# Kernel optimization log

Hardware: AMD Instinct MI355X
Metric: run time of the kernel (lower is better)

Reference implementation:

```python
import jax, jax.numpy as jnp
import numpy as np

NU, NB, NI = 50000, 20000, 100000
D = 64
NUM_LAYERS = 2
CORE_K = 3
PAD = NI  # padding index for bundle_items
BATCH, NCAND = 2048, 2
MAXDEG = 50
E_UB, E_UI, E_BI = 800000, 1000000, 1200000
N_UB, N_UI, N_BI = NU + NB, NU + NI, NB + NI


def setup_inputs():
    key = jax.random.key(0)
    ks = jax.random.split(key, 24)
    f = jnp.float32
    inp = {
        'users_feature': jax.random.normal(ks[0], (NU, D), f) * 0.1,
        'bundles_feature': jax.random.normal(ks[1], (NB, D), f) * 0.1,
        'items_feature': jax.random.normal(ks[2], (NI, D), f) * 0.1,
        'mlp_core_w1': jax.random.normal(ks[3], (2, 32), f) * 0.1,
        'mlp_core_b1': jnp.zeros((32,), f),
        'mlp_core_w2': jax.random.normal(ks[4], (32, 1), f) * 0.1,
        'mlp_core_b2': jnp.zeros((1,), f),
        'mlp_syn_w1': jax.random.normal(ks[5], (2 * D, D), f) * 0.05,
        'mlp_syn_b1': jnp.zeros((D,), f),
        'mlp_syn_w2': jax.random.normal(ks[6], (D, D), f) * 0.05,
        'mlp_syn_b2': jnp.zeros((D,), f),
        'ub_val': jax.random.uniform(ks[7], (E_UB,), f) * 0.2,
        'ui_val': jax.random.uniform(ks[8], (E_UI,), f) * 0.2,
        'bi_val': jax.random.uniform(ks[9], (E_BI,), f) * 0.2,
        'users': jax.random.randint(ks[10], (BATCH,), 0, NU),
        'bundles': jax.random.randint(ks[11], (BATCH, NCAND), 0, NB),
        'ub_row': jax.random.randint(ks[12], (E_UB,), 0, N_UB, jnp.int32),
        'ub_col': jax.random.randint(ks[13], (E_UB,), 0, N_UB, jnp.int32),
        'ui_row': jax.random.randint(ks[14], (E_UI,), 0, N_UI, jnp.int32),
        'ui_col': jax.random.randint(ks[15], (E_UI,), 0, N_UI, jnp.int32),
        'bi_row': jax.random.randint(ks[16], (E_BI,), 0, N_BI, jnp.int32),
        'bi_col': jax.random.randint(ks[17], (E_BI,), 0, N_BI, jnp.int32),
        'bundle_items': jax.random.randint(ks[18], (NB, MAXDEG), 0, NI + 1),
    }
    return inp


def spmm(row, col, val, x):
    # y = A @ x for COO sparse A: gather source rows, scale, scatter-add to dest rows
    return jax.ops.segment_sum(val[:, None] * x[col], row, num_segments=x.shape[0])


def propagate(row, col, val, feat_a, feat_b):
    f = jnp.concatenate([feat_a, feat_b], axis=0)
    acc = f
    for _ in range(NUM_LAYERS):
        f = spmm(row, col, val, f)
        acc = acc + f
    m = acc / (NUM_LAYERS + 1)  # mean over hop outputs
    return m[:feat_a.shape[0]], m[feat_a.shape[0]:]


def core_fringe_scores(users, bundles, reps, bundle_items,
                       cw1, cb1, cw2, cb2, sw1, sb1, sw2, sb2):
    UB_u, UB_b, UI_u, UI_i, BI_b, BI_i = reps
    B, C = bundles.shape
    users_exp = jnp.repeat(users, C)            # [B*C]
    bundles_flat = bundles.reshape(-1)          # [B*C]
    bbi = bundle_items[bundles_flat]            # [B*C, M]
    mask = bbi != PAD
    zero = jnp.zeros((1, D), UI_i.dtype)
    items_ui = jnp.concatenate([UI_i, zero], 0)[bbi]  # [B*C, M, D]
    items_bi = jnp.concatenate([BI_i, zero], 0)[bbi]
    u_ui = UI_u[users_exp]                      # [B*C, D]
    b_bi = BI_b[bundles_flat]
    r_UI = jnp.einsum('nd,nmd->nm', u_ui, items_ui)
    r_BI = jnp.einsum('nd,nmd->nm', b_bi, items_bi)
    x = jnp.stack([r_UI, r_BI], axis=-1)        # [B*C, M, 2]
    h = jax.nn.relu(x @ cw1 + cb1)              # dropout omitted (eval-mode determinism)
    logits = (h @ cw2 + cb2)[..., 0]
    logits = jnp.where(mask, logits, -jnp.inf)
    pi = jax.nn.softmax(logits, axis=1)
    k = min(CORE_K, bbi.shape[1])
    topv, topi = jax.lax.top_k(pi, k)
    topp = topv / (topv.sum(axis=1, keepdims=True) + 1e-10)
    core_emb = jnp.take_along_axis(items_ui, topi[:, :, None], axis=1)
    h_core = (core_emb * topp[:, :, None]).sum(axis=1)
    n = pi.shape[0]
    is_core = jnp.zeros(pi.shape, bool).at[jnp.arange(n)[:, None], topi].set(True)
    is_fringe = mask & ~is_core
    fr = is_fringe[:, :, None].astype(items_ui.dtype)
    fringe_sum = (items_ui * fr).sum(axis=1)
    fringe_cnt = jnp.maximum(is_fringe.sum(axis=1, keepdims=True).astype(items_ui.dtype), 1.0)
    h_fringe = fringe_sum / fringe_cnt
    syn = jnp.concatenate([h_core, h_fringe], axis=1)
    phi = jax.nn.relu(syn @ sw1 + sb1) @ sw2 + sb2
    hat_e_BI = h_core + phi
    user_final = jnp.concatenate([u_ui, UB_u[users_exp]], axis=1)
    bundle_final = jnp.concatenate([UB_b[bundles_flat], hat_e_BI], axis=1)
    scores = (user_final * bundle_final).sum(axis=1)
    return scores.reshape(B, C)


def reference(users_feature, bundles_feature, items_feature,
              mlp_core_w1, mlp_core_b1, mlp_core_w2, mlp_core_b2,
              mlp_syn_w1, mlp_syn_b1, mlp_syn_w2, mlp_syn_b2,
              ub_val, ui_val, bi_val,
              users, bundles, ub_row, ub_col, ui_row, ui_col,
              bi_row, bi_col, bundle_items):
    UB_u, UB_b = propagate(ub_row, ub_col, ub_val, users_feature, bundles_feature)
    UI_u, UI_i = propagate(ui_row, ui_col, ui_val, users_feature, items_feature)
    BI_b, BI_i = propagate(bi_row, bi_col, bi_val, bundles_feature, items_feature)
    reps = (UB_u, UB_b, UI_u, UI_i, BI_b, BI_i)
    scores = core_fringe_scores(users, bundles, reps, bundle_items,
                                mlp_core_w1, mlp_core_b1, mlp_core_w2, mlp_core_b2,
                                mlp_syn_w1, mlp_syn_b1, mlp_syn_w2, mlp_syn_b2)
    # BPR loss: -log(sigmoid(pos - neg)) == softplus(neg - pos)
    bpr_loss = jnp.mean(jax.nn.softplus(scores[:, 1:] - scores[:, 0:1]))
    return bpr_loss
```

## Files before the change

kernel.cpp:

```cpp
#include <hip/hip_runtime.h>
#include <math.h>

constexpr int D = 64;
constexpr int NU = 50000, NB = 20000, NI = 100000;
constexpr int BATCH = 2048, NCAND = 2, MAXDEG = 50, CORE_K = 3;
constexpr int PAD_IDX = NI;
constexpr int N_UB = NU + NB, N_UI = NU + NI, N_BI = NB + NI;
constexpr int N_TOT = N_UB + N_UI + N_BI;
constexpr int OFF1 = N_UB;
constexpr int OFF2 = N_UB + N_UI;
constexpr int CAP = 48;
constexpr float VAL_SCALE = 16383.0f / 0.2f;
constexpr float VAL_INV   = 0.2f / 16383.0f;

constexpr int GB_BASE = NU;
constexpr int GI_BASE = NU + NB;
constexpr int NGF = NU + NB + NI;

constexpr int BSHIFT = 9;
constexpr int BROWS  = 1 << BSHIFT;
constexpr int NBUCK  = (N_TOT + BROWS - 1) >> BSHIFT;
constexpr int BCAP   = 6144;
constexpr int P1_EPT = 16;
constexpr int P1_TPB = 256;
constexpr int P1_EPB = P1_EPT * P1_TPB;

constexpr int L2_NCB = BATCH * NCAND;
constexpr int L2_SLOTS = 2 * NI + 2 * BATCH + 2 * L2_NCB;
constexpr int S_UBU = 2 * NI;
constexpr int S_UIU = 2 * NI + BATCH;
constexpr int S_UBB = 2 * NI + 2 * BATCH;
constexpr int S_BIB = S_UBB + L2_NCB;

constexpr int MARK_A_BLOCKS = (L2_NCB * MAXDEG + 255) / 256;
constexpr int MARK_B_ROWS   = BATCH + L2_NCB;

__device__ __forceinline__ float wave_sum64(float v) {
#pragma unroll
    for (int off = 32; off > 0; off >>= 1) v += __shfl_down(v, off);
    return v;
}

__device__ __forceinline__ float bflo(unsigned u) { return __uint_as_float(u << 16); }
__device__ __forceinline__ float bfhi(unsigned u) { return __uint_as_float(u & 0xFFFF0000u); }
__device__ __forceinline__ unsigned short f2bf(float f) {
    unsigned u = __float_as_uint(f);
    u += 0x7FFF + ((u >> 16) & 1);
    return (unsigned short)(u >> 16);
}
__device__ __forceinline__ unsigned pack2(float a, float b) {
    return (unsigned)f2bf(a) | ((unsigned)f2bf(b) << 16);
}
__device__ __forceinline__ float bf1(const unsigned short* p) {
    return __uint_as_float(((unsigned)*p) << 16);
}

__device__ __forceinline__ void edge_decode(unsigned u, int& col, float& v) {
    col = (int)(u & 0x3FFFFu);
    v = (float)(u >> 18) * VAL_INV;
}

__global__ __launch_bounds__(256) void k_bin1cvt(
    const int* __restrict__ r0, const int* __restrict__ c0,
    const float* __restrict__ v0,
    const int* __restrict__ r1, const int* __restrict__ c1,
    const float* __restrict__ v1,
    const int* __restrict__ r2, const int* __restrict__ c2,
    const float* __restrict__ v2,
    int e0, int e1, int e2, int nb1,
    int* __restrict__ bcnt, uint2* __restrict__ stage,
    const float* __restrict__ uf, const float* __restrict__ bf,
    const float* __restrict__ itf, unsigned short* __restrict__ gt) {
    const int t = threadIdx.x;
    if ((int)blockIdx.x >= nb1) {
        size_t i = (size_t)(blockIdx.x - nb1) * 256 + t;
        if (i >= (size_t)NGF * 16) return;
        int row = (int)(i >> 4);
        int q = ((int)i & 15) * 4;
        const float* src;
        if (row < GB_BASE)      src = uf  + (size_t)row * D;
        else if (row < GI_BASE) src = bf  + (size_t)(row - GB_BASE) * D;
        else                    src = itf + (size_t)(row - GI_BASE) * D;
        float4 v = *(const float4*)(src + q);
        ushort4 o;
        o.x = f2bf(v.x); o.y = f2bf(v.y); o.z = f2bf(v.z); o.w = f2bf(v.w);
        *(ushort4*)(gt + (size_t)row * D + q) = o;
        return;
    }
    __shared__ int s_hist[NBUCK];
    __shared__ unsigned s_base[NBUCK];
    __shared__ uint2 s_ed[P1_EPB];
    const int etot = e0 + e1 + e2;
    const int i0 = blockIdx.x * P1_EPB + t;
    for (int l = t; l < NBUCK; l += P1_TPB) s_hist[l] = 0;
    __syncthreads();
#pragma unroll
    for (int k = 0; k < P1_EPT; ++k) {
        int i = i0 + k * P1_TPB;
        uint2 ed = make_uint2(0u, 0xFFFFFFFFu);
        if (i < etot) {
            int r, g; float v;
            if (i < e0)           { r = r0[i]; g = c0[i]; v = v0[i]; }
            else if (i < e0 + e1) { int j = i - e0; r = r1[j] + OFF1;
                                    int c = c1[j]; g = (c < NU) ? c : c + NB; v = v1[j]; }
            else                  { int j = i - e0 - e1; r = r2[j] + OFF2;
                                    g = c2[j] + NU; v = v2[j]; }
            unsigned q = (unsigned)fminf(v * VAL_SCALE + 0.5f, 16383.0f);
            int lo = atomicAdd(&s_hist[r >> BSHIFT], 1);
            ed = make_uint2((q << 18) | (unsigned)g,
                            (unsigned)r | ((unsigned)lo << 19));
        }
        s_ed[k * P1_TPB + t] = ed;
    }
    __syncthreads();
    for (int l = t; l < NBUCK; l += P1_TPB)
        s_base[l] = (unsigned)atomicAdd(&bcnt[l], s_hist[l]);
    __syncthreads();
#pragma unroll
    for (int k = 0; k < P1_EPT; ++k) {
        uint2 e = s_ed[k * P1_TPB + t];
        if (e.y == 0xFFFFFFFFu) continue;
        unsigned r = e.y & 0x7FFFFu;
        unsigned b = r >> BSHIFT;
        unsigned slot = s_base[b] + (e.y >> 19);
        if (slot < (unsigned)BCAP)
            stage[(size_t)b * BCAP + slot] = make_uint2(e.x, r);
    }
}

__global__ __launch_bounds__(1024) void k_bin2(
    const int* __restrict__ bcnt, const uint2* __restrict__ stage,
    int* __restrict__ cnt, unsigned* __restrict__ cv) {
    __shared__ unsigned lcv[BROWS][CAP];
    __shared__ int s_c[BROWS];
    const int b = blockIdx.x;
    const int t = threadIdx.x;
    if (t < BROWS) s_c[t] = 0;
    __syncthreads();
    int nb = bcnt[b]; if (nb > BCAP) nb = BCAP;
    const uint2* sp = stage + (size_t)b * BCAP;
    const int rbase = b << BSHIFT;
    for (int i = t; i < nb; i += 1024) {
        uint2 e = sp[i];
        int rl = (int)e.y - rbase;
        int slot = atomicAdd(&s_c[rl], 1);
        if (slot < CAP) lcv[rl][slot] = e.x;
    }
    __syncthreads();
    if (t < BROWS && rbase + t < N_TOT) cnt[rbase + t] = s_c[t];
    const int g16 = t >> 4;
    const int l16 = t & 15;
#pragma unroll 1
    for (int rl = g16; rl < BROWS; rl += 64) {
        int r = rbase + rl;
        if (r >= N_TOT) continue;
        int deg = s_c[rl]; if (deg > CAP) deg = CAP;
        if (deg == 0) continue;
        int nwords = (deg + 15) & ~15;
        if (l16 * 4 < nwords) {
            uint4 w = *(const uint4*)&lcv[rl][l16 * 4];
            *(uint4*)(cv + (size_t)r * CAP + l16 * 4) = w;
        }
    }
}

__global__ __launch_bounds__(256) void k_mark(
    const int* __restrict__ users, const int* __restrict__ bundles,
    const int* __restrict__ bundle_items,
    const int* __restrict__ cnt, const unsigned* __restrict__ cv,
    unsigned char* __restrict__ fS, unsigned char* __restrict__ f1,
    unsigned char* __restrict__ f2) {
    const int bid = blockIdx.x, t = threadIdx.x;
    if (bid < MARK_A_BLOCKS) {
        int i = bid * 256 + t;
        if (i < L2_NCB * MAXDEG) {
            int it = bundle_items[(size_t)bundles[i / MAXDEG] * MAXDEG + (i % MAXDEG)];
            if (it != PAD_IDX) fS[it] = 1;
        }
        return;
    }
    int q = (bid - MARK_A_BLOCKS) * 256 + t;
    if (q >= MARK_B_ROWS) return;
    int r; unsigned char* f;
    if (q < BATCH) { r = OFF1 + users[q];          f = f1; }
    else           { r = OFF2 + bundles[q - BATCH]; f = f2; }
    int deg = cnt[r]; if (deg > CAP) deg = CAP;
    const unsigned* ce = cv + (size_t)r * CAP;
    for (int j = 0; j < deg; ++j) {
        int g = (int)(ce[j] & 0x3FFFFu);
        if (g >= GI_BASE) f[g - GI_BASE] = 1;
    }
}

__global__ __launch_bounds__(256) void k_spmm_l1(
    const int* __restrict__ cnt, const unsigned* __restrict__ cv,
    const unsigned short* __restrict__ gt,
    const unsigned char* __restrict__ f1, const unsigned char* __restrict__ f2,
    unsigned short* __restrict__ y1) {
    int r = blockIdx.x * 32 + (threadIdx.x >> 3);
    int t = threadIdx.x & 7;
    if (r >= N_TOT) return;
    if (r >= OFF1 + NU && r < OFF2) { if (!f1[r - OFF1 - NU]) return; }
    else if (r >= OFF2 + NB)        { if (!f2[r - OFF2 - NB]) return; }
    int deg = cnt[r]; if (deg > CAP) deg = CAP;
    const unsigned* ce = cv + (size_t)r * CAP;
    float a[8];
#pragma unroll
    for (int k = 0; k < 8; ++k) a[k] = 0.f;
    int j = 0;
    for (; j + 3 < deg; j += 4) {
        int c[4]; float v[4]; uint4 u[4];
#pragma unroll
        for (int k = 0; k < 4; ++k) edge_decode(ce[j + k], c[k], v[k]);
#pragma unroll
        for (int k = 0; k < 4; ++k)
            u[k] = *(const uint4*)(gt + (((size_t)c[k]) << 6) + t * 8);
#pragma unroll
        for (int k = 0; k < 4; ++k) {
            a[0] = fmaf(v[k], bflo(u[k].x), a[0]); a[1] = fmaf(v[k], bfhi(u[k].x), a[1]);
            a[2] = fmaf(v[k], bflo(u[k].y), a[2]); a[3] = fmaf(v[k], bfhi(u[k].y), a[3]);
            a[4] = fmaf(v[k], bflo(u[k].z), a[4]); a[5] = fmaf(v[k], bfhi(u[k].z), a[5]);
            a[6] = fmaf(v[k], bflo(u[k].w), a[6]); a[7] = fmaf(v[k], bfhi(u[k].w), a[7]);
        }
    }
    for (; j < deg; ++j) {
        int c0; float v0;
        edge_decode(ce[j], c0, v0);
        uint4 u0 = *(const uint4*)(gt + (((size_t)c0) << 6) + t * 8);
        a[0] = fmaf(v0, bflo(u0.x), a[0]); a[1] = fmaf(v0, bfhi(u0.x), a[1]);
        a[2] = fmaf(v0, bflo(u0.y), a[2]); a[3] = fmaf(v0, bfhi(u0.y), a[3]);
        a[4] = fmaf(v0, bflo(u0.z), a[4]); a[5] = fmaf(v0, bfhi(u0.z), a[5]);
        a[6] = fmaf(v0, bflo(u0.w), a[6]); a[7] = fmaf(v0, bfhi(u0.w), a[7]);
    }
    uint4 o;
    o.x = pack2(a[0], a[1]); o.y = pack2(a[2], a[3]);
    o.z = pack2(a[4], a[5]); o.w = pack2(a[6], a[7]);
    *(uint4*)(y1 + ((size_t)r << 6) + t * 8) = o;
}

__global__ __launch_bounds__(256) void k_spmm_l2(
    const int* __restrict__ cnt, const unsigned* __restrict__ cv,
    const int* __restrict__ users, const int* __restrict__ bundles,
    const unsigned short* __restrict__ y1, const unsigned short* __restrict__ gt,
    const unsigned char* __restrict__ fS,
    unsigned short* __restrict__ xc) {
    int s = blockIdx.x * 32 + (threadIdx.x >> 3);
    int t = threadIdx.x & 7;
    if (s >= L2_SLOTS) return;
    int r, g, sec;
    if (s < NI)                { if (!fS[s]) return;
                                 r = OFF1 + NU + s;        g = GI_BASE + s;        sec = 1; }
    else if (s < 2 * NI)       { int i = s - NI; if (!fS[i]) return;
                                 r = OFF2 + NB + i;        g = GI_BASE + i;        sec = 2; }
    else {
        int q = s - 2 * NI;
        if (q < BATCH)            { int u = users[q];             r = u;         g = u;            sec = 0; }
        else if (q < 2 * BATCH)   { int u = users[q - BATCH];     r = OFF1 + u;  g = u;            sec = 1; }
        else if (q < S_BIB - 2 * NI) { int b = bundles[q - 2 * BATCH];
                                    r = NU + b;    g = GB_BASE + b;  sec = 0; }
        else                      { int b = bundles[q - (S_BIB - 2 * NI)];
                                    r = OFF2 + b;  g = GB_BASE + b;  sec = 2; }
    }
    auto y1row = [&](int gg) -> int {
        if (sec == 0) return gg;
        if (sec == 2) return OFF2 - GB_BASE + gg;
        return OFF1 + ((gg < NU) ? gg : gg - NB);
    };
    int deg = cnt[r]; if (deg > CAP) deg = CAP;
    const unsigned* ce = cv + (size_t)r * CAP;
    float a[8];
#pragma unroll
    for (int k = 0; k < 8; ++k) a[k] = 0.f;
    int j = 0;
    for (; j + 3 < deg; j += 4) {
        int c[4]; float v[4]; uint4 u[4];
#pragma unroll
        for (int k = 0; k < 4; ++k) edge_decode(ce[j + k], c[k], v[k]);
#pragma unroll
        for (int k = 0; k < 4; ++k)
            u[k] = *(const uint4*)(y1 + (((size_t)y1row(c[k])) << 6) + t * 8);
#pragma unroll
        for (int k = 0; k < 4; ++k) {
            a[0] = fmaf(v[k], bflo(u[k].x), a[0]); a[1] = fmaf(v[k], bfhi(u[k].x), a[1]);
            a[2] = fmaf(v[k], bflo(u[k].y), a[2]); a[3] = fmaf(v[k], bfhi(u[k].y), a[3]);
            a[4] = fmaf(v[k], bflo(u[k].z), a[4]); a[5] = fmaf(v[k], bfhi(u[k].z), a[5]);
            a[6] = fmaf(v[k], bflo(u[k].w), a[6]); a[7] = fmaf(v[k], bfhi(u[k].w), a[7]);
        }
    }
    for (; j < deg; ++j) {
        int c0; float v0;
        edge_decode(ce[j], c0, v0);
        uint4 u0 = *(const uint4*)(y1 + (((size_t)y1row(c0)) << 6) + t * 8);
        a[0] = fmaf(v0, bflo(u0.x), a[0]); a[1] = fmaf(v0, bfhi(u0.x), a[1]);
        a[2] = fmaf(v0, bflo(u0.y), a[2]); a[3] = fmaf(v0, bfhi(u0.y), a[3]);
        a[4] = fmaf(v0, bflo(u0.z), a[4]); a[5] = fmaf(v0, bfhi(u0.z), a[5]);
        a[6] = fmaf(v0, bflo(u0.w), a[6]); a[7] = fmaf(v0, bfhi(u0.w), a[7]);
    }
    uint4 fx = *(const uint4*)(gt + ((size_t)g << 6) + t * 8);
    uint4 yx = *(const uint4*)(y1 + ((size_t)r << 6) + t * 8);
    constexpr float k3 = 1.0f / 3.0f;
    float o[8];
    o[0] = (bflo(fx.x) + bflo(yx.x) + a[0]) * k3;
    o[1] = (bfhi(fx.x) + bfhi(yx.x) + a[1]) * k3;
    o[2] = (bflo(fx.y) + bflo(yx.y) + a[2]) * k3;
    o[3] = (bfhi(fx.y) + bfhi(yx.y) + a[3]) * k3;
    o[4] = (bflo(fx.z) + bflo(yx.z) + a[4]) * k3;
    o[5] = (bfhi(fx.z) + bfhi(yx.z) + a[5]) * k3;
    o[6] = (bflo(fx.w) + bflo(yx.w) + a[6]) * k3;
    o[7] = (bfhi(fx.w) + bfhi(yx.w) + a[7]) * k3;
    uint4 w;
    w.x = pack2(o[0], o[1]); w.y = pack2(o[2], o[3]);
    w.z = pack2(o[4], o[5]); w.w = pack2(o[6], o[7]);
    *(uint4*)(xc + ((size_t)s << 6) + t * 8) = w;
}

__global__ __launch_bounds__(256) void k_score(
    const int* __restrict__ bundles,
    const int* __restrict__ bundle_items,
    const unsigned short* __restrict__ xc,
    const float* __restrict__ cw1, const float* __restrict__ cb1,
    const float* __restrict__ cw2, const float* __restrict__ cb2,
    const float* __restrict__ sw1, const float* __restrict__ sb1,
    const float* __restrict__ sw2, const float* __restrict__ sb2,
    float* __restrict__ accum, unsigned* __restrict__ tick,
    float* __restrict__ out) {
    const int t  = threadIdx.x;
    const int wv = t >> 6;
    const int ln = t & 63;
    const int n  = blockIdx.x * 4 + wv;
    const int g8 = ln >> 3;
    const int l8 = ln & 7;
    const int uq = n >> 1;
    const int b = bundles[n];

    __shared__ unsigned sh_it[4][MAXDEG][32];
    __shared__ float sh_r[4][2][MAXDEG];
    __shared__ float sh_syn[4][2 * D];
    __shared__ float sh_h1[4][D];
    __shared__ float sh_sc[4];

    int my_idx = (ln < MAXDEG) ? bundle_items[(size_t)b * MAXDEG + ln] : PAD_IDX;
    unsigned long long vmask = __ballot(my_idx != PAD_IDX);

    uint4 ufr = *(const uint4*)(xc + (((size_t)(S_UIU + uq)) << 6) + l8 * 8);
    uint4 bfr = *(const uint4*)(xc + (((size_t)(S_BIB + n)) << 6) + l8 * 8);
    float uf0 = bflo(ufr.x), uf1 = bfhi(ufr.x), uf2 = bflo(ufr.y), uf3 = bfhi(ufr.y);
    float uf4 = bflo(ufr.z), uf5 = bfhi(ufr.z), uf6 = bflo(ufr.w), uf7 = bfhi(ufr.w);
    float bf0 = bflo(bfr.x), bf1_ = bfhi(bfr.x), bf2 = bflo(bfr.y), bf3 = bfhi(bfr.y);
    float bf4 = bflo(bfr.z), bf5 = bfhi(bfr.z), bf6 = bflo(bfr.w), bf7 = bfhi(bfr.w);

    for (int iter = 0; iter < (MAXDEG + 7) / 8; ++iter) {
        int m = iter * 8 + g8;
        if (m >= MAXDEG) continue;
        int it = __shfl(my_idx, m);
        uint4 iu = make_uint4(0, 0, 0, 0);
        float pu = 0.f, pb = 0.f;
        if (it != PAD_IDX) {
            iu = *(const uint4*)(xc + (((size_t)it) << 6) + l8 * 8);
            uint4 ib = *(const uint4*)(xc + (((size_t)(NI + it)) << 6) + l8 * 8);
            pu = uf0 * bflo(iu.x) + uf1 * bfhi(iu.x) + uf2 * bflo(iu.y) + uf3 * bfhi(iu.y)
               + uf4 * bflo(iu.z) + uf5 * bfhi(iu.z) + uf6 * bflo(iu.w) + uf7 * bfhi(iu.w);
            pb = bf0 * bflo(ib.x) + bf1_ * bfhi(ib.x) + bf2 * bflo(ib.y) + bf3 * bfhi(ib.y)
               + bf4 * bflo(ib.z) + bf5 * bfhi(ib.z) + bf6 * bflo(ib.w) + bf7 * bfhi(ib.w);
        }
        *(uint4*)&sh_it[wv][m][l8 * 4] = iu;
#pragma unroll
        for (int off = 4; off > 0; off >>= 1) {
            pu += __shfl_down(pu, off, 8);
            pb += __shfl_down(pb, off, 8);
        }
        if (l8 == 0) { sh_r[wv][0][m] = pu; sh_r[wv][1][m] = pb; }
    }
    __builtin_amdgcn_wave_barrier();

    float logit = -INFINITY;
    if (ln < MAXDEG && my_idx != PAD_IDX) {
        float rU = sh_r[wv][0][ln], rB = sh_r[wv][1][ln];
        float acc = cb2[0];
#pragma unroll
        for (int j = 0; j < 32; ++j) {
            float h = fmaf(rU, cw1[j], fmaf(rB, cw1[32 + j], cb1[j]));
            h = fmaxf(h, 0.f);
            acc = fmaf(h, cw2[j], acc);
        }
        logit = acc;
    }

    float mx = logit;
#pragma unroll
    for (int off = 32; off > 0; off >>= 1) mx = fmaxf(mx, __shfl_xor(mx, off));
    float e = expf(logit - mx);
    float sm = e;
#pragma unroll
    for (int off = 32; off > 0; off >>= 1) sm += __shfl_xor(sm, off);
    float p = e / sm;

    int ti[CORE_K]; float tp[CORE_K];
    float vsel = p;
#pragma unroll
    for (int k = 0; k < CORE_K; ++k) {
        float vv = vsel; int ii = ln;
#pragma unroll
        for (int off = 32; off > 0; off >>= 1) {
            float v2 = __shfl_xor(vv, off);
            int   i2 = __shfl_xor(ii, off);
            if (v2 > vv || (v2 == vv && i2 < ii)) { vv = v2; ii = i2; }
        }
        ti[k] = ii; tp[k] = vv;
        if (ln == ii) vsel = -1.f;
    }
    float tinv = 1.f / (tp[0] + tp[1] + tp[2] + 1e-10f);
    tp[0] *= tinv; tp[1] *= tinv; tp[2] *= tinv;

    int ti0 = ti[0], ti1 = ti[1], ti2 = ti[2];
    const int ui_w = ln >> 1;
    const bool hi = (ln & 1);
    auto feat = [&](int m) -> float {
        unsigned w = sh_it[wv][m][ui_w];
        return hi ? bfhi(w) : bflo(w);
    };
    float hcore = feat(ti0) * tp[0] + feat(ti1) * tp[1] + feat(ti2) * tp[2];
    float fsum = 0.f;
#pragma unroll 10
    for (int m = 0; m < MAXDEG; ++m) fsum += feat(m);
    int fcnt = __popcll(vmask);
#pragma unroll
    for (int k = 0; k < CORE_K; ++k) {
        if ((vmask >> ti[k]) & 1ull) { fsum -= feat(ti[k]); fcnt--; }
    }
    float hfr = fsum / fmaxf((float)fcnt, 1.f);
    sh_syn[wv][ln] = hcore;
    sh_syn[wv][D + ln] = hfr;
    __builtin_amdgcn_wave_barrier();

    float h1 = sb1[ln];
#pragma unroll 8
    for (int k0 = 0; k0 < 32; ++k0) {
        float4 s4 = *(const float4*)&sh_syn[wv][k0 * 4];
        h1 = fmaf(s4.x, sw1[(k0 * 4 + 0) * D + ln], h1);
        h1 = fmaf(s4.y, sw1[(k0 * 4 + 1) * D + ln], h1);
        h1 = fmaf(s4.z, sw1[(k0 * 4 + 2) * D + ln], h1);
        h1 = fmaf(s4.w, sw1[(k0 * 4 + 3) * D + ln], h1);
    }
    sh_h1[wv][ln] = fmaxf(h1, 0.f);
    __builtin_amdgcn_wave_barrier();
    float phi = sb2[ln];
#pragma unroll 8
    for (int k0 = 0; k0 < 16; ++k0) {
        float4 s4 = *(const float4*)&sh_h1[wv][k0 * 4];
        phi = fmaf(s4.x, sw2[(k0 * 4 + 0) * D + ln], phi);
        phi = fmaf(s4.y, sw2[(k0 * 4 + 1) * D + ln], phi);
        phi = fmaf(s4.z, sw2[(k0 * 4 + 2) * D + ln], phi);
        phi = fmaf(s4.w, sw2[(k0 * 4 + 3) * D + ln], phi);
    }

    float hat = hcore + phi;
    float uui = bf1(xc + (((size_t)(S_UIU + uq)) << 6) + ln);
    float ubu = bf1(xc + (((size_t)(S_UBU + uq)) << 6) + ln);
    float ubb = bf1(xc + (((size_t)(S_UBB + n)) << 6) + ln);
    float part = wave_sum64(uui * ubb + ubu * hat);
    if (ln == 0) sh_sc[wv] = part;

    __syncthreads();
    if (t == 0) {
        float x01 = sh_sc[1] - sh_sc[0];
        float x23 = sh_sc[3] - sh_sc[2];
        float spv = fmaxf(x01, 0.f) + log1pf(expf(-fabsf(x01)))
                  + fmaxf(x23, 0.f) + log1pf(expf(-fabsf(x23)));
        atomicAdd(accum, spv * (1.0f / (float)BATCH));
        __threadfence();
        unsigned old = atomicAdd(tick, 1u);
        if (old == gridDim.x - 1) {
            __threadfence();
            float total = atomicAdd(accum, 0.0f);
            out[0] = total;
        }
    }
}

extern "C" void kernel_launch(void* const* d_in, const int* in_sizes, int n_in,
                              void* d_out, int out_size, void* d_ws, size_t ws_size,
                              hipStream_t stream) {
    const float* users_feature   = (const float*)d_in[0];
    const float* bundles_feature = (const float*)d_in[1];
    const float* items_feature   = (const float*)d_in[2];
    const float* cw1 = (const float*)d_in[3];
    const float* cb1 = (const float*)d_in[4];
    const float* cw2 = (const float*)d_in[5];
    const float* cb2 = (const float*)d_in[6];
    const float* sw1 = (const float*)d_in[7];
    const float* sb1 = (const float*)d_in[8];
    const float* sw2 = (const float*)d_in[9];
    const float* sb2 = (const float*)d_in[10];
    const float* ub_val = (const float*)d_in[11];
    const float* ui_val = (const float*)d_in[12];
    const float* bi_val = (const float*)d_in[13];
    const int* users   = (const int*)d_in[14];
    const int* bundles = (const int*)d_in[15];
    const int* ub_row = (const int*)d_in[16];
    const int* ub_col = (const int*)d_in[17];
    const int* ui_row = (const int*)d_in[18];
    const int* ui_col = (const int*)d_in[19];
    const int* bi_row = (const int*)d_in[20];
    const int* bi_col = (const int*)d_in[21];
    const int* bundle_items = (const int*)d_in[22];
    const int E_UB = in_sizes[11], E_UI = in_sizes[12], E_BI = in_sizes[13];
    const int E_TOT = E_UB + E_UI + E_BI;

    float* ws = (float*)d_ws;
    size_t off = 0;
    unsigned short* gt  = (unsigned short*)(ws + off); off += (size_t)NGF * 32;
    unsigned short* y1b = (unsigned short*)(ws + off); off += (size_t)N_TOT * 32;
    unsigned* cv  = (unsigned*)(ws + off); off += (size_t)N_TOT * CAP;
    uint2* stage = (uint2*)(ws + off);
    unsigned short* xc = (unsigned short*)(ws + off);
    off += (size_t)NBUCK * BCAP * 2;
    int*   bcnt   = (int*)(ws + off); off += NBUCK;
    unsigned* tick = (unsigned*)(ws + off); off += 1;
    float* accum  = (float*)(ws + off); off += 1;
    unsigned char* fS = (unsigned char*)(ws + off); off += NI / 4;
    unsigned char* f1 = (unsigned char*)(ws + off); off += NI / 4;
    unsigned char* f2 = (unsigned char*)(ws + off); off += NI / 4;
    int*   cnt    = (int*)(ws + off); off += N_TOT;
    if (ws_size < off * sizeof(float)) return;

    hipMemsetAsync(bcnt, 0, (NBUCK + 2) * sizeof(int) + 3 * NI, stream);

    const int nb1 = (E_TOT + P1_EPB - 1) / P1_EPB;
    const int ncvt = (int)(((size_t)NGF * 16 + 255) / 256);
    k_bin1cvt<<<nb1 + ncvt, P1_TPB, 0, stream>>>(
        ub_row, ub_col, ub_val, ui_row, ui_col, ui_val, bi_row, bi_col, bi_val,
        E_UB, E_UI, E_BI, nb1, bcnt, stage,
        users_feature, bundles_feature, items_feature, gt);

    k_bin2<<<NBUCK, 1024, 0, stream>>>(bcnt, stage, cnt, cv);

    const int nmarkB = (MARK_B_ROWS + 255) / 256;
    k_mark<<<MARK_A_BLOCKS + nmarkB, 256, 0, stream>>>(
        users, bundles, bundle_items, cnt, cv, fS, f1, f2);

    k_spmm_l1<<<(N_TOT + 31) / 32, 256, 0, stream>>>(cnt, cv, gt, f1, f2, y1b);

    k_spmm_l2<<<(L2_SLOTS + 31) / 32, 256, 0, stream>>>(
        cnt, cv, users, bundles, y1b, gt, fS, xc);

    k_score<<<(BATCH * NCAND) / 4, 256, 0, stream>>>(
        bundles, bundle_items, xc,
        cw1, cb1, cw2, cb2, sw1, sb1, sw2, sb2,
        accum, tick, (float*)d_out);
}
```

Measured before the change: 331.9 us.

## Fold marking kernel into binning kernels and halve edges per thread

Removes the separate k_mark launch. Item-set marking and user/bundle batch flags now run as extra blocks of the first binning kernel, and neighbor marking of batch rows happens inside k_bin2 from shared-memory adjacency. Edges per thread in the first pass drop from 16 to 8, which doubles the number of binning blocks. The aim is to save a launch plus a global re-read of cv/cnt, at the cost of serial per-row marking loops in k_bin2 and more global atomics on the bucket counters.

```diff
diff --git a/kernel.cpp b/kernel.cpp
--- a/kernel.cpp
+++ b/kernel.cpp
@@ -21,7 +21,7 @@
 constexpr int BROWS  = 1 << BSHIFT;
 constexpr int NBUCK  = (N_TOT + BROWS - 1) >> BSHIFT;
 constexpr int BCAP   = 6144;
-constexpr int P1_EPT = 16;
+constexpr int P1_EPT = 8;
 constexpr int P1_TPB = 256;
 constexpr int P1_EPB = P1_EPT * P1_TPB;
 
@@ -33,7 +33,7 @@
 constexpr int S_BIB = S_UBB + L2_NCB;
 
 constexpr int MARK_A_BLOCKS = (L2_NCB * MAXDEG + 255) / 256;
-constexpr int MARK_B_ROWS   = BATCH + L2_NCB;
+constexpr int MARK_D_BLOCKS = (BATCH + L2_NCB + 255) / 256;
 
 __device__ __forceinline__ float wave_sum64(float v) {
 #pragma unroll
@@ -67,13 +67,32 @@
     const float* __restrict__ v1,
     const int* __restrict__ r2, const int* __restrict__ c2,
     const float* __restrict__ v2,
-    int e0, int e1, int e2, int nb1,
+    int e0, int e1, int e2, int nb1, int nb2, int nb3,
     int* __restrict__ bcnt, uint2* __restrict__ stage,
     const float* __restrict__ uf, const float* __restrict__ bf,
-    const float* __restrict__ itf, unsigned short* __restrict__ gt) {
+    const float* __restrict__ itf, unsigned short* __restrict__ gt,
+    const int* __restrict__ users, const int* __restrict__ bundles,
+    const int* __restrict__ bundle_items,
+    unsigned char* __restrict__ fS, unsigned char* __restrict__ du,
+    unsigned char* __restrict__ db) {
     const int t = threadIdx.x;
-    if ((int)blockIdx.x >= nb1) {
-        size_t i = (size_t)(blockIdx.x - nb1) * 256 + t;
+    const int bid = (int)blockIdx.x;
+    if (bid >= nb3) {
+        int q = (bid - nb3) * 256 + t;
+        if (q < BATCH) du[users[q]] = 1;
+        else if (q < BATCH + L2_NCB) db[bundles[q - BATCH]] = 1;
+        return;
+    }
+    if (bid >= nb2) {
+        int i = (bid - nb2) * 256 + t;
+        if (i < L2_NCB * MAXDEG) {
+            int it = bundle_items[(size_t)bundles[i / MAXDEG] * MAXDEG + (i % MAXDEG)];
+            if (it != PAD_IDX) fS[it] = 1;
+        }
+        return;
+    }
+    if (bid >= nb1) {
+        size_t i = (size_t)(bid - nb1) * 256 + t;
         if (i >= (size_t)NGF * 16) return;
         int row = (int)(i >> 4);
         int q = ((int)i & 15) * 4;
@@ -91,7 +110,7 @@
     __shared__ unsigned s_base[NBUCK];
     __shared__ uint2 s_ed[P1_EPB];
     const int etot = e0 + e1 + e2;
-    const int i0 = blockIdx.x * P1_EPB + t;
+    const int i0 = bid * P1_EPB + t;
     for (int l = t; l < NBUCK; l += P1_TPB) s_hist[l] = 0;
     __syncthreads();
 #pragma unroll
@@ -130,7 +149,9 @@
 
 __global__ __launch_bounds__(1024) void k_bin2(
     const int* __restrict__ bcnt, const uint2* __restrict__ stage,
-    int* __restrict__ cnt, unsigned* __restrict__ cv) {
+    const unsigned char* __restrict__ du, const unsigned char* __restrict__ db,
+    int* __restrict__ cnt, unsigned* __restrict__ cv,
+    unsigned char* __restrict__ f1, unsigned char* __restrict__ f2) {
     __shared__ unsigned lcv[BROWS][CAP];
     __shared__ int s_c[BROWS];
     const int b = blockIdx.x;
@@ -148,6 +169,19 @@
     }
     __syncthreads();
     if (t < BROWS && rbase + t < N_TOT) cnt[rbase + t] = s_c[t];
+    if (t < BROWS) {
+        int r = rbase + t;
+        unsigned char* f = nullptr;
+        if (r >= OFF1 && r < OFF1 + NU)      { if (du[r - OFF1]) f = f1; }
+        else if (r >= OFF2 && r < OFF2 + NB) { if (db[r - OFF2]) f = f2; }
+        if (f) {
+            int deg = s_c[t]; if (deg > CAP) deg = CAP;
+            for (int j = 0; j < deg; ++j) {
+                int g = (int)(lcv[t][j] & 0x3FFFFu);
+                if (g >= GI_BASE) f[g - GI_BASE] = 1;
+            }
+        }
+    }
     const int g16 = t >> 4;
     const int l16 = t & 15;
 #pragma unroll 1
@@ -161,34 +195,6 @@
             uint4 w = *(const uint4*)&lcv[rl][l16 * 4];
             *(uint4*)(cv + (size_t)r * CAP + l16 * 4) = w;
         }
-    }
-}
-
-__global__ __launch_bounds__(256) void k_mark(
-    const int* __restrict__ users, const int* __restrict__ bundles,
-    const int* __restrict__ bundle_items,
-    const int* __restrict__ cnt, const unsigned* __restrict__ cv,
-    unsigned char* __restrict__ fS, unsigned char* __restrict__ f1,
-    unsigned char* __restrict__ f2) {
-    const int bid = blockIdx.x, t = threadIdx.x;
-    if (bid < MARK_A_BLOCKS) {
-        int i = bid * 256 + t;
-        if (i < L2_NCB * MAXDEG) {
-            int it = bundle_items[(size_t)bundles[i / MAXDEG] * MAXDEG + (i % MAXDEG)];
-            if (it != PAD_IDX) fS[it] = 1;
-        }
-        return;
-    }
-    int q = (bid - MARK_A_BLOCKS) * 256 + t;
-    if (q >= MARK_B_ROWS) return;
-    int r; unsigned char* f;
-    if (q < BATCH) { r = OFF1 + users[q];          f = f1; }
-    else           { r = OFF2 + bundles[q - BATCH]; f = f2; }
-    int deg = cnt[r]; if (deg > CAP) deg = CAP;
-    const unsigned* ce = cv + (size_t)r * CAP;
-    for (int j = 0; j < deg; ++j) {
-        int g = (int)(ce[j] & 0x3FFFFu);
-        if (g >= GI_BASE) f[g - GI_BASE] = 1;
     }
 }
 
@@ -521,23 +527,24 @@
     unsigned char* fS = (unsigned char*)(ws + off); off += NI / 4;
     unsigned char* f1 = (unsigned char*)(ws + off); off += NI / 4;
     unsigned char* f2 = (unsigned char*)(ws + off); off += NI / 4;
+    unsigned char* du = (unsigned char*)(ws + off); off += NU / 4;
+    unsigned char* db = (unsigned char*)(ws + off); off += NB / 4;
     int*   cnt    = (int*)(ws + off); off += N_TOT;
     if (ws_size < off * sizeof(float)) return;
 
-    hipMemsetAsync(bcnt, 0, (NBUCK + 2) * sizeof(int) + 3 * NI, stream);
+    hipMemsetAsync(bcnt, 0, (NBUCK + 2) * sizeof(int) + 3 * NI + NU + NB, stream);
 
     const int nb1 = (E_TOT + P1_EPB - 1) / P1_EPB;
     const int ncvt = (int)(((size_t)NGF * 16 + 255) / 256);
-    k_bin1cvt<<<nb1 + ncvt, P1_TPB, 0, stream>>>(
+    const int nb2 = nb1 + ncvt;
+    const int nb3 = nb2 + MARK_A_BLOCKS;
+    k_bin1cvt<<<nb3 + MARK_D_BLOCKS, P1_TPB, 0, stream>>>(
         ub_row, ub_col, ub_val, ui_row, ui_col, ui_val, bi_row, bi_col, bi_val,
-        E_UB, E_UI, E_BI, nb1, bcnt, stage,
-        users_feature, bundles_feature, items_feature, gt);
-
-    k_bin2<<<NBUCK, 1024, 0, stream>>>(bcnt, stage, cnt, cv);
-
-    const int nmarkB = (MARK_B_ROWS + 255) / 256;
-    k_mark<<<MARK_A_BLOCKS + nmarkB, 256, 0, stream>>>(
-        users, bundles, bundle_items, cnt, cv, fS, f1, f2);
+        E_UB, E_UI, E_BI, nb1, nb2, nb3, bcnt, stage,
+        users_feature, bundles_feature, items_feature, gt,
+        users, bundles, bundle_items, fS, du, db);
+
+    k_bin2<<<NBUCK, 1024, 0, stream>>>(bcnt, stage, du, db, cnt, cv, f1, f2);
 
     k_spmm_l1<<<(N_TOT + 31) / 32, 256, 0, stream>>>(cnt, cv, gt, f1, f2, y1b);
 
```

New measurement: 335.7 us. No clear change (+1.1%).
